# Kernel optimization log

Hardware: AMD Instinct MI355X
Metric: run time of the kernel (lower is better)

## Reference

```python
import jax, jax.numpy as jnp
import numpy as np

NEG_SLOPE = 0.01  # F.leaky_relu default
EPS = 1e-6


def setup_inputs() -> dict:
    key = jax.random.key(0)
    k1, k2, k3, k4 = jax.random.split(key, 4)
    N, E, IN, OUT = 100000, 1600000, 128, 64
    x = jax.random.normal(k1, (N, IN), dtype=jnp.float32)
    W = jax.random.normal(k2, (OUT, IN), dtype=jnp.float32) * (1.0 / np.sqrt(IN))
    a = jax.random.uniform(k3, (2 * OUT,), dtype=jnp.float32)  # uniform [0,1) as in init
    edge_index = jax.random.randint(k4, (2, E), 0, N, dtype=jnp.int64)
    return {"x": x, "W": W, "a": a, "edge_index": edge_index}


def reference(x, W, a, edge_index):
    N = x.shape[0]
    out_f = W.shape[0]
    # add self loops: append (i, i) for every node
    loops = jnp.arange(N, dtype=edge_index.dtype)
    ei = jnp.concatenate([edge_index, jnp.stack([loops, loops])], axis=1)
    src, dst = ei[0], ei[1]

    messages = x @ W.T                      # [N, out]
    h_src = messages[src]                   # [E', out]
    h_dst = messages[dst]                   # [E', out]

    # e = cat([h_dst, h_src]) . a  == h_dst.a[:out] + h_src.a[out:]
    e = h_dst @ a[:out_f] + h_src @ a[out_f:]
    e = jnp.where(e >= 0, e, NEG_SLOPE * e)  # leaky_relu
    w = jnp.exp(e)                           # unnormalized edge weights

    denom = jax.ops.segment_sum(w, dst, num_segments=N)                     # [N]
    agg = jax.ops.segment_sum(h_src * w[:, None], dst, num_segments=N)      # [N, out]
    return agg / jnp.clip(denom, EPS)[:, None]
```

## Files before the change

kernel.cpp:

```cpp
#include <hip/hip_runtime.h>
#include <hip/hip_bf16.h>

#define IN_F 128
#define OUT_F 64
#define NEG 0.01f
#define LDSP 132

#define BUCKET_N 256
#define EPB 8192
#define CAP 48
#define MAXB 512
#define MAXSLAB 512

__device__ __forceinline__ float leaky_exp(float e) {
    e = (e >= 0.f) ? e : NEG * e;
    return expf(e);
}

__device__ __forceinline__ float b2f(unsigned int hi16_as_low) {
    return __uint_as_float(hi16_as_low);
}

__global__ __launch_bounds__(256) void gemm_msg_kernel(
    const float* __restrict__ x, const float* __restrict__ W,
    const float* __restrict__ a,
    __hip_bfloat16* __restrict__ msg, float* __restrict__ alpha,
    float* __restrict__ beta, int N)
{
    __shared__ float xs[64 * LDSP];
    __shared__ float Ws[64 * LDSP];
    const int tid = threadIdx.x;
    const int base = blockIdx.x * 64;

#pragma unroll
    for (int t = 0; t < 8; ++t) {
        int i = tid + t * 256;
        int c = i >> 5, k4 = i & 31;
        float4 wv = ((const float4*)W)[i];
        *(float4*)&Ws[c * LDSP + k4 * 4] = wv;
    }
#pragma unroll
    for (int t = 0; t < 8; ++t) {
        int i = tid + t * 256;
        int r = i >> 5, k4 = i & 31;
        int row = base + r;
        float4 xv = make_float4(0.f, 0.f, 0.f, 0.f);
        if (row < N) xv = ((const float4*)x)[(size_t)row * (IN_F / 4) + k4];
        *(float4*)&xs[r * LDSP + k4 * 4] = xv;
    }
    __syncthreads();

    const int tx = tid & 15;
    const int ty = tid >> 4;
    const float* xrow = &xs[(ty * 4) * LDSP];
    const float* wrow = &Ws[(tx * 4) * LDSP];

    float acc[4][4] = {};
    for (int k = 0; k < IN_F; k += 4) {
        float4 xv[4], wv[4];
#pragma unroll
        for (int i = 0; i < 4; ++i) xv[i] = *(const float4*)&xrow[i * LDSP + k];
#pragma unroll
        for (int i = 0; i < 4; ++i) wv[i] = *(const float4*)&wrow[i * LDSP + k];
#pragma unroll
        for (int ri = 0; ri < 4; ++ri)
#pragma unroll
            for (int ci = 0; ci < 4; ++ci) {
                acc[ri][ci] += xv[ri].x * wv[ci].x;
                acc[ri][ci] += xv[ri].y * wv[ci].y;
                acc[ri][ci] += xv[ri].z * wv[ci].z;
                acc[ri][ci] += xv[ri].w * wv[ci].w;
            }
    }

    float a_lo[4], a_hi[4];
#pragma unroll
    for (int ci = 0; ci < 4; ++ci) {
        a_lo[ci] = a[tx * 4 + ci];
        a_hi[ci] = a[OUT_F + tx * 4 + ci];
    }

#pragma unroll
    for (int ri = 0; ri < 4; ++ri) {
        int row = base + ty * 4 + ri;
        if (row < N) {
            union { ushort4 u; __hip_bfloat16 h[4]; } pk;
            pk.h[0] = __float2bfloat16(acc[ri][0]);
            pk.h[1] = __float2bfloat16(acc[ri][1]);
            pk.h[2] = __float2bfloat16(acc[ri][2]);
            pk.h[3] = __float2bfloat16(acc[ri][3]);
            *(ushort4*)&msg[(size_t)row * OUT_F + tx * 4] = pk.u;
        }
        float pa = acc[ri][0] * a_lo[0] + acc[ri][1] * a_lo[1] +
                   acc[ri][2] * a_lo[2] + acc[ri][3] * a_lo[3];
        float pb = acc[ri][0] * a_hi[0] + acc[ri][1] * a_hi[1] +
                   acc[ri][2] * a_hi[2] + acc[ri][3] * a_hi[3];
#pragma unroll
        for (int off = 1; off < 16; off <<= 1) {
            pa += __shfl_xor(pa, off);
            pb += __shfl_xor(pb, off);
        }
        if (tx == 0 && row < N) { alpha[row] = pa; beta[row] = pb; }
    }
}

__global__ __launch_bounds__(512) void partition_kernel(
    const int* __restrict__ src, const int* __restrict__ dst,
    int* __restrict__ counts, unsigned int* __restrict__ cells,
    int* __restrict__ bucket_tot, int E, int B, int NBLKP)
{
    __shared__ int cnt_s[MAXB];
    for (int i = threadIdx.x; i < B; i += 512) cnt_s[i] = 0;
    __syncthreads();

    const size_t pbase = (size_t)blockIdx.x * B;

#pragma unroll
    for (int u = 0; u < 4; ++u) {
        const int i4 = blockIdx.x * 2048 + u * 512 + threadIdx.x;
        const int e0 = i4 * 4;
        if (e0 + 3 < E) {
            int4 s4 = ((const int4*)src)[i4];
            int4 d4 = ((const int4*)dst)[i4];
            int b0 = d4.x >> 8, b1 = d4.y >> 8, b2 = d4.z >> 8, b3 = d4.w >> 8;
            int r0 = atomicAdd(&cnt_s[b0], 1);
            int r1 = atomicAdd(&cnt_s[b1], 1);
            int r2 = atomicAdd(&cnt_s[b2], 1);
            int r3 = atomicAdd(&cnt_s[b3], 1);
            if (r0 < CAP) cells[(pbase + b0) * CAP + r0] =
                (unsigned)s4.x | ((unsigned)(d4.x & 255) << 20);
            if (r1 < CAP) cells[(pbase + b1) * CAP + r1] =
                (unsigned)s4.y | ((unsigned)(d4.y & 255) << 20);
            if (r2 < CAP) cells[(pbase + b2) * CAP + r2] =
                (unsigned)s4.z | ((unsigned)(d4.z & 255) << 20);
            if (r3 < CAP) cells[(pbase + b3) * CAP + r3] =
                (unsigned)s4.w | ((unsigned)(d4.w & 255) << 20);
        } else {
            for (int e = e0; e < E && e < e0 + 4; ++e) {
                int s = src[e], d = dst[e];
                int b = d >> 8;
                int r = atomicAdd(&cnt_s[b], 1);
                if (r < CAP) cells[(pbase + b) * CAP + r] =
                    (unsigned)s | ((unsigned)(d & 255) << 20);
            }
        }
    }
    __syncthreads();
    for (int i = threadIdx.x; i < B; i += 512) {
        int c = min(cnt_s[i], CAP);
        counts[(size_t)i * NBLKP + blockIdx.x] = c;
        atomicAdd(&bucket_tot[i], c);
    }
}

__global__ __launch_bounds__(512) void bucket_scan_kernel(
    const int* __restrict__ bucket_tot, int* __restrict__ bucket_base,
    int* __restrict__ offs, int N, int B)
{
    __shared__ int tmp[512];
    const int t = threadIdx.x;
    int v = (t < B) ? bucket_tot[t] : 0;
    tmp[t] = v;
    __syncthreads();
#pragma unroll
    for (int d = 1; d < 512; d <<= 1) {
        int add = (t >= d) ? tmp[t - d] : 0;
        __syncthreads();
        tmp[t] += add;
        __syncthreads();
    }
    if (t < B) bucket_base[t] = tmp[t] - v;
    if (t == 511) offs[N] = tmp[511];
}

__global__ __launch_bounds__(512) void compact_kernel(
    const int* __restrict__ counts, const unsigned int* __restrict__ cells,
    const int* __restrict__ bucket_base,
    const float* __restrict__ alpha, const float* __restrict__ beta,
    int* __restrict__ offs, int2* __restrict__ edges,
    int N, int B, int NBLK, int NBLKP)
{
    __shared__ int cnt_l[MAXSLAB];
    __shared__ int hist[BUCKET_N];
    __shared__ int scan_s[BUCKET_N];
    __shared__ int cursor[BUCKET_N];
    __shared__ float alpha_s[BUCKET_N];
    const int b = blockIdx.x;
    const int tid = threadIdx.x;
    const int wave = tid >> 6, lane = tid & 63;

    for (int i = tid; i < NBLK; i += 512) cnt_l[i] = counts[(size_t)b * NBLKP + i];
    if (tid < BUCKET_N) {
        hist[tid] = 0;
        int g = b * BUCKET_N + tid;
        alpha_s[tid] = (g < N) ? alpha[g] : 0.f;
    }
    __syncthreads();

    for (int sl = wave; sl < NBLK; sl += 8) {
        int c = cnt_l[sl];
        if (lane < c) {
            unsigned v = cells[((size_t)sl * B + b) * CAP + lane];
            atomicAdd(&hist[v >> 20], 1);
        }
    }
    __syncthreads();

    int hv = 0;
    if (tid < BUCKET_N) { hv = hist[tid]; scan_s[tid] = hv; }
    __syncthreads();
#pragma unroll
    for (int d = 1; d < BUCKET_N; d <<= 1) {
        int add = (tid < BUCKET_N && tid >= d) ? scan_s[tid - d] : 0;
        __syncthreads();
        if (tid < BUCKET_N) scan_s[tid] += add;
        __syncthreads();
    }
    const int gbase = bucket_base[b];
    if (tid < BUCKET_N) {
        int excl = scan_s[tid] - hv;
        cursor[tid] = excl;
        int g = b * BUCKET_N + tid;
        if (g < N) offs[g] = gbase + excl;
    }
    __syncthreads();

    for (int sl = wave; sl < NBLK; sl += 8) {
        int c = cnt_l[sl];
        if (lane < c) {
            unsigned v = cells[((size_t)sl * B + b) * CAP + lane];
            int s = v & 0xFFFFF;
            int l = v >> 20;
            float w = leaky_exp(alpha_s[l] + beta[s]);
            int pos = atomicAdd(&cursor[l], 1);
            edges[gbase + pos] = make_int2(s, __float_as_int(w));
        }
    }
}

__global__ __launch_bounds__(256) void aggregate_kernel(
    const int* __restrict__ offs, const int2* __restrict__ edges,
    const __hip_bfloat16* __restrict__ msg,
    const float* __restrict__ alpha, const float* __restrict__ beta,
    float* __restrict__ out, int N)
{
    const int node = blockIdx.x * 4 + (threadIdx.x >> 6);
    if (node >= N) return;
    const int lane = threadIdx.x & 63;
    const int g = lane & 15;
    const int u = lane >> 4;

    const unsigned short* msp = (const unsigned short*)msg;

    float acc0 = 0.f, acc1 = 0.f, acc2 = 0.f, acc3 = 0.f, den = 0.f;

    {
        const float ws = leaky_exp(alpha[node] + beta[node]);
        ushort4 mv = *(const ushort4*)&msp[(size_t)node * OUT_F + 4 * g];
        float wsel = (u == 0) ? ws : 0.f;
        acc0 += wsel * b2f((unsigned)mv.x << 16);
        acc1 += wsel * b2f((unsigned)mv.y << 16);
        acc2 += wsel * b2f((unsigned)mv.z << 16);
        acc3 += wsel * b2f((unsigned)mv.w << 16);
        den  += wsel;
    }

    const int st = offs[node], en = offs[node + 1];
    for (int j = st; j < en; j += 16) {
#pragma unroll
        for (int uu = 0; uu < 4; ++uu) {
            int idx = j + uu * 4 + u;
            int ii = min(idx, en - 1);
            int2 e = edges[ii];
            float w = (idx < en) ? __int_as_float(e.y) : 0.f;
            ushort4 mv = *(const ushort4*)&msp[(size_t)e.x * OUT_F + 4 * g];
            acc0 += w * b2f((unsigned)mv.x << 16);
            acc1 += w * b2f((unsigned)mv.y << 16);
            acc2 += w * b2f((unsigned)mv.z << 16);
            acc3 += w * b2f((unsigned)mv.w << 16);
            den  += w;
        }
    }

#pragma unroll
    for (int off = 16; off <= 32; off <<= 1) {
        acc0 += __shfl_xor(acc0, off);
        acc1 += __shfl_xor(acc1, off);
        acc2 += __shfl_xor(acc2, off);
        acc3 += __shfl_xor(acc3, off);
        den  += __shfl_xor(den, off);
    }

    if (lane < 16) {
        float dn = 1.f / fmaxf(den, 1e-6f);
        *(float4*)&out[(size_t)node * OUT_F + 4 * lane] =
            make_float4(acc0 * dn, acc1 * dn, acc2 * dn, acc3 * dn);
    }
}

extern "C" void kernel_launch(void* const* d_in, const int* in_sizes, int n_in,
                              void* d_out, int out_size, void* d_ws, size_t ws_size,
                              hipStream_t stream) {
    const float* x  = (const float*)d_in[0];
    const float* W  = (const float*)d_in[1];
    const float* a  = (const float*)d_in[2];
    const int*   ei = (const int*)d_in[3];
    float* out = (float*)d_out;

    const int IN = in_sizes[1] / OUT_F;
    const int N  = in_sizes[0] / IN;
    const int E  = in_sizes[3] / 2;
    const int B  = (N + BUCKET_N - 1) / BUCKET_N;
    const int NBLK  = (E + EPB - 1) / EPB;
    const int NBLKP = (NBLK + 3) & ~3;

    auto align16 = [](size_t v) { return (v + 15) & ~(size_t)15; };
    char* p = (char*)d_ws;
    __hip_bfloat16* msg = (__hip_bfloat16*)p; p += align16((size_t)N * OUT_F * 2);
    float* alpha  = (float*)p; p += align16((size_t)N * 4);
    float* beta   = (float*)p; p += align16((size_t)N * 4);
    int*   counts = (int*)p;   p += align16((size_t)B * NBLKP * 4);
    unsigned int* cells = (unsigned int*)p; p += align16((size_t)NBLK * B * CAP * 4);
    int*   btot   = (int*)p;   p += align16((size_t)B * 4);
    int*   bbase  = (int*)p;   p += align16((size_t)B * 4);
    int*   offs   = (int*)p;   p += align16((size_t)(N + 1) * 4);
    int2*  edges  = (int2*)p;  p += align16((size_t)E * 8);

    const int* esrc = ei;
    const int* edst = ei + E;

    hipMemsetAsync(btot, 0, (size_t)B * 4, stream);

    gemm_msg_kernel<<<(N + 63) / 64, 256, 0, stream>>>(x, W, a, msg, alpha, beta, N);
    partition_kernel<<<NBLK, 512, 0, stream>>>(esrc, edst, counts, cells,
                                               btot, E, B, NBLKP);
    bucket_scan_kernel<<<1, 512, 0, stream>>>(btot, bbase, offs, N, B);
    compact_kernel<<<B, 512, 0, stream>>>(counts, cells, bbase, alpha, beta,
                                          offs, edges, N, B, NBLK, NBLKP);
    aggregate_kernel<<<(N + 3) / 4, 256, 0, stream>>>(offs, edges, msg,
                                                      alpha, beta, out, N);
}
```

Before: 160.4 us.

## Fold self-loop edges into CSR, pack alpha/beta, transpose W in LDS

Self-loop edges are now written into the compacted edge list by the compact kernel, and the bucket scan reserves one slot per node for them. This removes the special self-loop prologue and the alpha/beta reads from the aggregate kernel. Alpha and beta are packed into one float2 array so each gather is a single load. The GEMM now stores W transposed in LDS, so the inner loop reads contiguous output columns. The cost is an extra N edges in the workspace and the compacted stream.

```diff
diff --git a/kernel.cpp b/kernel.cpp
--- a/kernel.cpp
+++ b/kernel.cpp
@@ -5,6 +5,7 @@
 #define OUT_F 64
 #define NEG 0.01f
 #define LDSP 132
+#define WTP  68
 
 #define BUCKET_N 256
 #define EPB 8192
@@ -17,27 +18,28 @@
     return expf(e);
 }
 
-__device__ __forceinline__ float b2f(unsigned int hi16_as_low) {
-    return __uint_as_float(hi16_as_low);
-}
+__device__ __forceinline__ float b2f(unsigned int v) { return __uint_as_float(v); }
 
 __global__ __launch_bounds__(256) void gemm_msg_kernel(
     const float* __restrict__ x, const float* __restrict__ W,
     const float* __restrict__ a,
-    __hip_bfloat16* __restrict__ msg, float* __restrict__ alpha,
-    float* __restrict__ beta, int N)
+    __hip_bfloat16* __restrict__ msg, float2* __restrict__ ab, int N)
 {
     __shared__ float xs[64 * LDSP];
-    __shared__ float Ws[64 * LDSP];
+    __shared__ float Wt[IN_F * WTP];
     const int tid = threadIdx.x;
     const int base = blockIdx.x * 64;
 
 #pragma unroll
     for (int t = 0; t < 8; ++t) {
         int i = tid + t * 256;
-        int c = i >> 5, k4 = i & 31;
-        float4 wv = ((const float4*)W)[i];
-        *(float4*)&Ws[c * LDSP + k4 * 4] = wv;
+        int o = i & 63;
+        int k4 = i >> 6;
+        float4 wv = ((const float4*)W)[o * (IN_F / 4) + k4];
+        Wt[(k4 * 4 + 0) * WTP + o] = wv.x;
+        Wt[(k4 * 4 + 1) * WTP + o] = wv.y;
+        Wt[(k4 * 4 + 2) * WTP + o] = wv.z;
+        Wt[(k4 * 4 + 3) * WTP + o] = wv.w;
     }
 #pragma unroll
     for (int t = 0; t < 8; ++t) {
@@ -53,23 +55,24 @@
     const int tx = tid & 15;
     const int ty = tid >> 4;
     const float* xrow = &xs[(ty * 4) * LDSP];
-    const float* wrow = &Ws[(tx * 4) * LDSP];
 
     float acc[4][4] = {};
     for (int k = 0; k < IN_F; k += 4) {
-        float4 xv[4], wv[4];
-#pragma unroll
-        for (int i = 0; i < 4; ++i) xv[i] = *(const float4*)&xrow[i * LDSP + k];
-#pragma unroll
-        for (int i = 0; i < 4; ++i) wv[i] = *(const float4*)&wrow[i * LDSP + k];
+        float xq[4][4], wq[4][4];
+#pragma unroll
+        for (int i = 0; i < 4; ++i)
+            *(float4*)xq[i] = *(const float4*)&xrow[i * LDSP + k];
+#pragma unroll
+        for (int j = 0; j < 4; ++j)
+            *(float4*)wq[j] = *(const float4*)&Wt[(k + j) * WTP + tx * 4];
 #pragma unroll
         for (int ri = 0; ri < 4; ++ri)
 #pragma unroll
             for (int ci = 0; ci < 4; ++ci) {
-                acc[ri][ci] += xv[ri].x * wv[ci].x;
-                acc[ri][ci] += xv[ri].y * wv[ci].y;
-                acc[ri][ci] += xv[ri].z * wv[ci].z;
-                acc[ri][ci] += xv[ri].w * wv[ci].w;
+                acc[ri][ci] += xq[ri][0] * wq[0][ci];
+                acc[ri][ci] += xq[ri][1] * wq[1][ci];
+                acc[ri][ci] += xq[ri][2] * wq[2][ci];
+                acc[ri][ci] += xq[ri][3] * wq[3][ci];
             }
     }
 
@@ -100,7 +103,7 @@
             pa += __shfl_xor(pa, off);
             pb += __shfl_xor(pb, off);
         }
-        if (tx == 0 && row < N) { alpha[row] = pa; beta[row] = pb; }
+        if (tx == 0 && row < N) ab[row] = make_float2(pa, pb);
     }
 }
 
@@ -159,7 +162,12 @@
 {
     __shared__ int tmp[512];
     const int t = threadIdx.x;
-    int v = (t < B) ? bucket_tot[t] : 0;
+    int v = 0;
+    if (t < B) {
+        int nodes = N - t * BUCKET_N;
+        nodes = max(0, min(BUCKET_N, nodes));
+        v = bucket_tot[t] + nodes;
+    }
     tmp[t] = v;
     __syncthreads();
 #pragma unroll
@@ -175,8 +183,7 @@
 
 __global__ __launch_bounds__(512) void compact_kernel(
     const int* __restrict__ counts, const unsigned int* __restrict__ cells,
-    const int* __restrict__ bucket_base,
-    const float* __restrict__ alpha, const float* __restrict__ beta,
+    const int* __restrict__ bucket_base, const float2* __restrict__ ab,
     int* __restrict__ offs, int2* __restrict__ edges,
     int N, int B, int NBLK, int NBLKP)
 {
@@ -190,10 +197,13 @@
     const int wave = tid >> 6, lane = tid & 63;
 
     for (int i = tid; i < NBLK; i += 512) cnt_l[i] = counts[(size_t)b * NBLKP + i];
+    float2 myab = make_float2(0.f, 0.f);
     if (tid < BUCKET_N) {
-        hist[tid] = 0;
         int g = b * BUCKET_N + tid;
-        alpha_s[tid] = (g < N) ? alpha[g] : 0.f;
+        bool valid = (g < N);
+        hist[tid] = valid ? 1 : 0;
+        if (valid) myab = ab[g];
+        alpha_s[tid] = myab.x;
     }
     __syncthreads();
 
@@ -219,9 +229,13 @@
     const int gbase = bucket_base[b];
     if (tid < BUCKET_N) {
         int excl = scan_s[tid] - hv;
-        cursor[tid] = excl;
         int g = b * BUCKET_N + tid;
-        if (g < N) offs[g] = gbase + excl;
+        if (g < N) {
+            offs[g] = gbase + excl;
+            float wself = leaky_exp(myab.x + myab.y);
+            edges[gbase + excl] = make_int2(g, __float_as_int(wself));
+            cursor[tid] = excl + 1;
+        }
     }
     __syncthreads();
 
@@ -231,7 +245,7 @@
             unsigned v = cells[((size_t)sl * B + b) * CAP + lane];
             int s = v & 0xFFFFF;
             int l = v >> 20;
-            float w = leaky_exp(alpha_s[l] + beta[s]);
+            float w = leaky_exp(alpha_s[l] + ab[s].y);
             int pos = atomicAdd(&cursor[l], 1);
             edges[gbase + pos] = make_int2(s, __float_as_int(w));
         }
@@ -241,7 +255,6 @@
 __global__ __launch_bounds__(256) void aggregate_kernel(
     const int* __restrict__ offs, const int2* __restrict__ edges,
     const __hip_bfloat16* __restrict__ msg,
-    const float* __restrict__ alpha, const float* __restrict__ beta,
     float* __restrict__ out, int N)
 {
     const int node = blockIdx.x * 4 + (threadIdx.x >> 6);
@@ -253,17 +266,6 @@
     const unsigned short* msp = (const unsigned short*)msg;
 
     float acc0 = 0.f, acc1 = 0.f, acc2 = 0.f, acc3 = 0.f, den = 0.f;
-
-    {
-        const float ws = leaky_exp(alpha[node] + beta[node]);
-        ushort4 mv = *(const ushort4*)&msp[(size_t)node * OUT_F + 4 * g];
-        float wsel = (u == 0) ? ws : 0.f;
-        acc0 += wsel * b2f((unsigned)mv.x << 16);
-        acc1 += wsel * b2f((unsigned)mv.y << 16);
-        acc2 += wsel * b2f((unsigned)mv.z << 16);
-        acc3 += wsel * b2f((unsigned)mv.w << 16);
-        den  += wsel;
-    }
 
     const int st = offs[node], en = offs[node + 1];
     for (int j = st; j < en; j += 16) {
@@ -317,26 +319,24 @@
     auto align16 = [](size_t v) { return (v + 15) & ~(size_t)15; };
     char* p = (char*)d_ws;
     __hip_bfloat16* msg = (__hip_bfloat16*)p; p += align16((size_t)N * OUT_F * 2);
-    float* alpha  = (float*)p; p += align16((size_t)N * 4);
-    float* beta   = (float*)p; p += align16((size_t)N * 4);
+    float2* ab    = (float2*)p; p += align16((size_t)N * 8);
     int*   counts = (int*)p;   p += align16((size_t)B * NBLKP * 4);
     unsigned int* cells = (unsigned int*)p; p += align16((size_t)NBLK * B * CAP * 4);
     int*   btot   = (int*)p;   p += align16((size_t)B * 4);
     int*   bbase  = (int*)p;   p += align16((size_t)B * 4);
     int*   offs   = (int*)p;   p += align16((size_t)(N + 1) * 4);
-    int2*  edges  = (int2*)p;  p += align16((size_t)E * 8);
+    int2*  edges  = (int2*)p;  p += align16((size_t)(E + N) * 8);
 
     const int* esrc = ei;
     const int* edst = ei + E;
 
     hipMemsetAsync(btot, 0, (size_t)B * 4, stream);
 
-    gemm_msg_kernel<<<(N + 63) / 64, 256, 0, stream>>>(x, W, a, msg, alpha, beta, N);
+    gemm_msg_kernel<<<(N + 63) / 64, 256, 0, stream>>>(x, W, a, msg, ab, N);
     partition_kernel<<<NBLK, 512, 0, stream>>>(esrc, edst, counts, cells,
                                                btot, E, B, NBLKP);
     bucket_scan_kernel<<<1, 512, 0, stream>>>(btot, bbase, offs, N, B);
-    compact_kernel<<<B, 512, 0, stream>>>(counts, cells, bbase, alpha, beta,
+    compact_kernel<<<B, 512, 0, stream>>>(counts, cells, bbase, ab,
                                           offs, edges, N, B, NBLK, NBLKP);
-    aggregate_kernel<<<(N + 3) / 4, 256, 0, stream>>>(offs, edges, msg,
-                                                      alpha, beta, out, N);
-}
+    aggregate_kernel<<<(N + 3) / 4, 256, 0, stream>>>(offs, edges, msg, out, N);
+}
```

Result: faster. 153.9 us (-4.0%).
